# Performance work log

Measured on AMD Instinct MI355X. Metric: run time of the kernel, lower is better.

## Reference

```python
import jax, jax.numpy as jnp
import numpy as np
import math

D_MODEL = 2048
NUM_HEADS = 16
D_K = D_MODEL // NUM_HEADS  # 128
THETA = 10000.0
BATCH = 2
SEQ = 2048


def setup_inputs() -> dict:
    key = jax.random.key(0)
    k1, k2, k3 = jax.random.split(key, 3)
    std_qkv = math.sqrt(2.0 / (D_MODEL + 3 * D_MODEL))
    std_o = math.sqrt(2.0 / (D_MODEL + D_MODEL))
    return {
        "x": jax.random.normal(k1, (BATCH, SEQ, D_MODEL), dtype=jnp.float32),
        "token_positions": jnp.arange(SEQ, dtype=jnp.int64 if jax.config.jax_enable_x64 else jnp.int32),
        "Wqkv": jax.random.normal(k2, (3 * D_MODEL, D_MODEL), dtype=jnp.float32) * std_qkv,
        "Wo": jax.random.normal(k3, (D_MODEL, D_MODEL), dtype=jnp.float32) * std_o,
    }


def _rope(x, positions):
    # x: [b, h, t, d_k]; interleaved even/odd rotation as in the torch module
    half = D_K // 2
    inv_freq = 1.0 / (THETA ** (jnp.arange(half, dtype=x.dtype) / half))
    ang = positions.astype(x.dtype)[:, None] * inv_freq[None, :]  # [t, half]
    sin, cos = jnp.sin(ang), jnp.cos(ang)                          # broadcast over b,h
    x_even, x_odd = x[..., 0::2], x[..., 1::2]
    rot_even = x_even * cos - x_odd * sin
    rot_odd = x_even * sin + x_odd * cos
    return jnp.stack([rot_even, rot_odd], axis=-1).reshape(x.shape)


def reference(x, token_positions, Wqkv, Wo):
    B, T, _ = x.shape
    qkv = x @ Wqkv.T                                  # [b, t, 3*d_model]
    q, k, v = jnp.split(qkv, 3, axis=-1)
    def to_heads(t):
        return t.reshape(B, T, NUM_HEADS, D_K).transpose(0, 2, 1, 3)  # b h t d
    q, k, v = to_heads(q), to_heads(k), to_heads(v)
    q = _rope(q, token_positions)
    k = _rope(k, token_positions)
    scale = 1.0 / math.sqrt(D_K)
    scores = jnp.einsum("bhqd,bhkd->bhqk", q, k) * scale
    causal = jnp.tril(jnp.ones((T, T), dtype=bool))
    scores = jnp.where(causal, scores, jnp.finfo(scores.dtype).min)
    attn = jax.nn.softmax(scores, axis=-1)
    out = jnp.einsum("bhqk,bhkd->bhqd", attn, v)
    out = out.transpose(0, 2, 1, 3).reshape(B, T, D_MODEL)
    return out @ Wo.T
```

## Files before the change

### kernel.cpp

```cpp
#include <hip/hip_runtime.h>
#include <math.h>
#include <stdint.h>

#define NHEADS 16
#define DK 128
#define TSEQ 2048
#define DMODEL 2048

typedef __attribute__((ext_vector_type(8))) short short8;
typedef __attribute__((ext_vector_type(4))) float floatx4;

__device__ __forceinline__ float bf2f(unsigned short h) {
    return __uint_as_float(((unsigned int)h) << 16);
}
__device__ __forceinline__ unsigned short f2bf(float f) {
    unsigned int u = __float_as_uint(f);
    u += 0x7FFFu + ((u >> 16) & 1u);
    return (unsigned short)(u >> 16);
}
__device__ __forceinline__ void async16(unsigned short* lds, const unsigned short* g) {
    __builtin_amdgcn_global_load_lds(
        (const __attribute__((address_space(1))) uint32_t*)g,
        (__attribute__((address_space(3))) uint32_t*)lds, 16, 0, 0);
}

#define NX8 1048576
#define NW8 1572864
#define NO8 524288
__global__ __launch_bounds__(256) void cast_all_bf16(
    const float* __restrict__ x, const float* __restrict__ wqkv, const float* __restrict__ wo,
    unsigned short* __restrict__ xb, unsigned short* __restrict__ wqkvb, unsigned short* __restrict__ wob)
{
    const int i = blockIdx.x * 256 + threadIdx.x;
    const float* src; unsigned short* dst; int k;
    if (i < NX8)            { src = x;    dst = xb;    k = i; }
    else if (i < NX8 + NW8) { src = wqkv; dst = wqkvb; k = i - NX8; }
    else                    { src = wo;   dst = wob;   k = i - NX8 - NW8; }
    const float4* p4 = reinterpret_cast<const float4*>(src) + 2 * (size_t)k;
    const float4 a = p4[0], b = p4[1];
    uint32_t w0 = (uint32_t)f2bf(a.x) | ((uint32_t)f2bf(a.y) << 16);
    uint32_t w1 = (uint32_t)f2bf(a.z) | ((uint32_t)f2bf(a.w) << 16);
    uint32_t w2 = (uint32_t)f2bf(b.x) | ((uint32_t)f2bf(b.y) << 16);
    uint32_t w3 = (uint32_t)f2bf(b.z) | ((uint32_t)f2bf(b.w) << 16);
    uint4 o; o.x = w0; o.y = w1; o.z = w2; o.w = w3;
    *reinterpret_cast<uint4*>(dst + 8 * (size_t)k) = o;
}

__global__ __launch_bounds__(256) void rope_table_kernel(
    const int* __restrict__ pos, float2* __restrict__ tab)
{
    const int idx = blockIdx.x * 256 + threadIdx.x;
    const int tt = idx >> 6, i = idx & 63;
    const double inv_freq = exp(-log(10000.0) * (double)i / 64.0);
    const double ang = (double)pos[tt] * inv_freq;
    tab[idx] = make_float2((float)cos(ang), (float)sin(ang));
}

__global__ __launch_bounds__(512, 1) void gemm_qkv_8ph(
    const unsigned short* __restrict__ A, const unsigned short* __restrict__ B,
    unsigned short* __restrict__ qkvb, unsigned short* __restrict__ vt,
    const float2* __restrict__ tab)
{
    const int K = DMODEL, N = 3 * DMODEL;
    __shared__ unsigned short As[2][256 * 64];
    __shared__ unsigned short Bs[2][192 * 64];

    const int t = threadIdx.x;
    const int lane = t & 63, w = t >> 6;
    const int wr = w >> 2, wc = w & 3;
    const int lr = lane & 15, hi = lane >> 4;

    const int bid = (int)blockIdx.x;
    const int xcd = bid & 7, local = bid >> 3;
    const int row0 = (local & 15) * 256;
    const int col0 = ((xcd << 2) | (local >> 4)) * 192;

    const int rr = t >> 3;
    const int cc = ((t & 7) ^ (rr & 7)) << 3;
    const unsigned short* aP = A + (size_t)(row0 + rr) * K + cc;
    const unsigned short* bP = B + (size_t)(col0 + rr) * K + cc;
    const size_t rstep = (size_t)64 * K;

    floatx4 acc[8][3];
#pragma unroll
    for (int m = 0; m < 8; m++)
#pragma unroll
        for (int n = 0; n < 3; n++)
#pragma unroll
            for (int e = 0; e < 4; e++) acc[m][n][e] = 0.f;

#define STAGE_A(nb, k0n) do { \
        async16(&As[nb][t * 8],          aP + (k0n)); \
        async16(&As[nb][(t + 512) * 8],  aP + rstep + (k0n)); \
        async16(&As[nb][(t + 1024) * 8], aP + 2 * rstep + (k0n)); \
        async16(&As[nb][(t + 1536) * 8], aP + 3 * rstep + (k0n)); \
    } while (0)
#define STAGE_B(nb, k0n) do { \
        async16(&Bs[nb][t * 8],          bP + (k0n)); \
        async16(&Bs[nb][(t + 512) * 8],  bP + rstep + (k0n)); \
        async16(&Bs[nb][(t + 1024) * 8], bP + 2 * rstep + (k0n)); \
    } while (0)

    const int NT = K >> 6;
    const int ch0 = (hi ^ (lr & 7)) * 8;
    const int ch1 = ((4 + hi) ^ (lr & 7)) * 8;

    short8 av0[4][2], av1[4][2], bv[3][2];

#define RD_A(dst, Ac, mh) do { \
        _Pragma("unroll") \
        for (int m = 0; m < 4; m++) { \
            const int ar = (wr * 128 + (mh) * 64 + m * 16 + lr) * 64; \
            dst[m][0] = *(const short8*)&(Ac)[ar + ch0]; \
            dst[m][1] = *(const short8*)&(Ac)[ar + ch1]; \
        } \
    } while (0)
#define RD_B(Bc) do { \
        _Pragma("unroll") \
        for (int n = 0; n < 3; n++) { \
            const int br = (wc * 48 + n * 16 + lr) * 64; \
            bv[n][0] = *(const short8*)&(Bc)[br + ch0]; \
            bv[n][1] = *(const short8*)&(Bc)[br + ch1]; \
        } \
    } while (0)

    STAGE_A(0, 0);
    STAGE_B(0, 0);
    asm volatile("s_waitcnt vmcnt(0)" ::: "memory");
    __builtin_amdgcn_s_barrier();
    RD_A(av0, &As[0][0], 0);
    RD_B(&Bs[0][0]);

    for (int kt = 0; kt < NT; ++kt) {
        const int cur = kt & 1;
        const unsigned short* __restrict__ Ac = &As[cur][0];
        const unsigned short* __restrict__ Bc = &Bs[cur][0];
        const unsigned short* __restrict__ An = &As[cur ^ 1][0];
        const unsigned short* __restrict__ Bn = &Bs[cur ^ 1][0];
        const bool more = (kt + 1 < NT);

        if (more) STAGE_A(cur ^ 1, (kt + 1) << 6);
        RD_A(av1, Ac, 1);
        asm volatile("s_waitcnt lgkmcnt(8)" ::: "memory");
        __builtin_amdgcn_sched_barrier(0);
        __builtin_amdgcn_s_setprio(1);
#pragma unroll
        for (int m = 0; m < 4; m++)
#pragma unroll
            for (int n = 0; n < 3; n++) {
                acc[m][n] = __builtin_amdgcn_mfma_f32_16x16x32_bf16(av0[m][0], bv[n][0], acc[m][n], 0, 0, 0);
                acc[m][n] = __builtin_amdgcn_mfma_f32_16x16x32_bf16(av0[m][1], bv[n][1], acc[m][n], 0, 0, 0);
            }
        __builtin_amdgcn_s_setprio(0);

        if (more) STAGE_B(cur ^ 1, (kt + 1) << 6);
        asm volatile("s_waitcnt lgkmcnt(0)" ::: "memory");
        __builtin_amdgcn_sched_barrier(0);
        __builtin_amdgcn_s_setprio(1);
#pragma unroll
        for (int m = 0; m < 4; m++)
#pragma unroll
            for (int n = 0; n < 3; n++) {
                acc[4 + m][n] = __builtin_amdgcn_mfma_f32_16x16x32_bf16(av1[m][0], bv[n][0], acc[4 + m][n], 0, 0, 0);
                acc[4 + m][n] = __builtin_amdgcn_mfma_f32_16x16x32_bf16(av1[m][1], bv[n][1], acc[4 + m][n], 0, 0, 0);
            }
        __builtin_amdgcn_s_setprio(0);

        if (more) {
            asm volatile("s_waitcnt vmcnt(0)" ::: "memory");
            __builtin_amdgcn_s_barrier();
            RD_A(av0, An, 0);
            RD_B(Bn);
        }
    }
#undef STAGE_A
#undef STAGE_B
#undef RD_A
#undef RD_B

    const int par = lr & 1;
#pragma unroll
    for (int mi = 0; mi < 8; mi++) {
        const int row = row0 + wr * 128 + mi * 16 + hi * 4;
        const int tt = row & (TSEQ - 1);
        const int bb = row >> 11;
#pragma unroll
        for (int ni = 0; ni < 3; ni++) {
            const int col = col0 + wc * 48 + ni * 16 + lr;
            if (col < 2 * DMODEL) {
                const int pi = (col & 127) >> 1;
#pragma unroll
                for (int j = 0; j < 4; j++) {
                    const float2 cs = tab[(tt + j) * 64 + pi];
                    const float v = acc[mi][ni][j];
                    const float p = __shfl_xor(v, 1, 64);
                    const float o = par ? (p * cs.y + v * cs.x)
                                        : (v * cs.x - p * cs.y);
                    qkvb[(size_t)(row + j) * N + col] = f2bf(o);
                }
            } else {
                const int vcol = col - 2 * DMODEL;
                const int h = vcol >> 7, d = vcol & 127;
                uint2 pw;
                pw.x = (uint32_t)f2bf(acc[mi][ni][0]) | ((uint32_t)f2bf(acc[mi][ni][1]) << 16);
                pw.y = (uint32_t)f2bf(acc[mi][ni][2]) | ((uint32_t)f2bf(acc[mi][ni][3]) << 16);
                *(uint2*)&vt[(size_t)((bb * NHEADS + h) * DK + d) * TSEQ + tt] = pw;
            }
        }
    }
}

__global__ __launch_bounds__(512, 1) void gemm_o_8ph(
    const unsigned short* __restrict__ A, const unsigned short* __restrict__ B,
    float* __restrict__ C)
{
    const int K = DMODEL, N = DMODEL;
    __shared__ unsigned short As[2][256 * 64];
    __shared__ unsigned short Bs[2][128 * 64];

    const int t = threadIdx.x;
    const int lane = t & 63, w = t >> 6;
    const int wr = w >> 2, wc = w & 3;
    const int lr = lane & 15, hi = lane >> 4;

    const int bid = (int)blockIdx.x;
    const int xcd = bid & 7, local = bid >> 3;
    const int row0 = (local & 15) * 256;
    const int col0 = ((xcd << 1) | (local >> 4)) * 128;

    const int rr = t >> 3;
    const int cc = ((t & 7) ^ (rr & 7)) << 3;
    const unsigned short* aP = A + (size_t)(row0 + rr) * K + cc;
    const unsigned short* bP = B + (size_t)(col0 + rr) * K + cc;
    const size_t rstep = (size_t)64 * K;

    floatx4 acc[8][2];
#pragma unroll
    for (int m = 0; m < 8; m++)
#pragma unroll
        for (int n = 0; n < 2; n++)
#pragma unroll
            for (int e = 0; e < 4; e++) acc[m][n][e] = 0.f;

#define STAGE_A(nb, k0n) do { \
        async16(&As[nb][t * 8],          aP + (k0n)); \
        async16(&As[nb][(t + 512) * 8],  aP + rstep + (k0n)); \
        async16(&As[nb][(t + 1024) * 8], aP + 2 * rstep + (k0n)); \
        async16(&As[nb][(t + 1536) * 8], aP + 3 * rstep + (k0n)); \
    } while (0)
#define STAGE_B(nb, k0n) do { \
        async16(&Bs[nb][t * 8],          bP + (k0n)); \
        async16(&Bs[nb][(t + 512) * 8],  bP + rstep + (k0n)); \
    } while (0)

    const int NT = K >> 6;
    const int ch0 = (hi ^ (lr & 7)) * 8;
    const int ch1 = ((4 + hi) ^ (lr & 7)) * 8;

    short8 av0[4][2], av1[4][2], bv[2][2];

#define RD_A(dst, Ac, mh) do { \
        _Pragma("unroll") \
        for (int m = 0; m < 4; m++) { \
            const int ar = (wr * 128 + (mh) * 64 + m * 16 + lr) * 64; \
            dst[m][0] = *(const short8*)&(Ac)[ar + ch0]; \
            dst[m][1] = *(const short8*)&(Ac)[ar + ch1]; \
        } \
    } while (0)
#define RD_B(Bc) do { \
        _Pragma("unroll") \
        for (int n = 0; n < 2; n++) { \
            const int br = (wc * 32 + n * 16 + lr) * 64; \
            bv[n][0] = *(const short8*)&(Bc)[br + ch0]; \
            bv[n][1] = *(const short8*)&(Bc)[br + ch1]; \
        } \
    } while (0)

    STAGE_A(0, 0);
    STAGE_B(0, 0);
    asm volatile("s_waitcnt vmcnt(0)" ::: "memory");
    __builtin_amdgcn_s_barrier();
    RD_A(av0, &As[0][0], 0);
    RD_B(&Bs[0][0]);

    for (int kt = 0; kt < NT; ++kt) {
        const int cur = kt & 1;
        const unsigned short* __restrict__ Ac = &As[cur][0];
        const unsigned short* __restrict__ An = &As[cur ^ 1][0];
        const unsigned short* __restrict__ Bn = &Bs[cur ^ 1][0];
        const bool more = (kt + 1 < NT);

        if (more) STAGE_A(cur ^ 1, (kt + 1) << 6);
        RD_A(av1, Ac, 1);
        asm volatile("s_waitcnt lgkmcnt(8)" ::: "memory");
        __builtin_amdgcn_sched_barrier(0);
        __builtin_amdgcn_s_setprio(1);
#pragma unroll
        for (int m = 0; m < 4; m++)
#pragma unroll
            for (int n = 0; n < 2; n++) {
                acc[m][n] = __builtin_amdgcn_mfma_f32_16x16x32_bf16(av0[m][0], bv[n][0], acc[m][n], 0, 0, 0);
                acc[m][n] = __builtin_amdgcn_mfma_f32_16x16x32_bf16(av0[m][1], bv[n][1], acc[m][n], 0, 0, 0);
            }
        __builtin_amdgcn_s_setprio(0);

        if (more) STAGE_B(cur ^ 1, (kt + 1) << 6);
        asm volatile("s_waitcnt lgkmcnt(0)" ::: "memory");
        __builtin_amdgcn_sched_barrier(0);
        __builtin_amdgcn_s_setprio(1);
#pragma unroll
        for (int m = 0; m < 4; m++)
#pragma unroll
            for (int n = 0; n < 2; n++) {
                acc[4 + m][n] = __builtin_amdgcn_mfma_f32_16x16x32_bf16(av1[m][0], bv[n][0], acc[4 + m][n], 0, 0, 0);
                acc[4 + m][n] = __builtin_amdgcn_mfma_f32_16x16x32_bf16(av1[m][1], bv[n][1], acc[4 + m][n], 0, 0, 0);
            }
        __builtin_amdgcn_s_setprio(0);

        if (more) {
            asm volatile("s_waitcnt vmcnt(0)" ::: "memory");
            __builtin_amdgcn_s_barrier();
            RD_A(av0, An, 0);
            RD_B(Bn);
        }
    }
#undef STAGE_A
#undef STAGE_B
#undef RD_A
#undef RD_B

#pragma unroll
    for (int mi = 0; mi < 8; mi++) {
        const int row = row0 + wr * 128 + mi * 16 + hi * 4;
#pragma unroll
        for (int ni = 0; ni < 2; ni++) {
            const int col = col0 + wc * 32 + ni * 16 + lr;
#pragma unroll
            for (int j = 0; j < 4; j++)
                C[(size_t)(row + j) * N + col] = acc[mi][ni][j];
        }
    }
}

__global__ __launch_bounds__(256, 2) void attn_mfma2_kernel(
    const unsigned short* __restrict__ qkvb, const unsigned short* __restrict__ vt,
    unsigned short* __restrict__ outb)
{
    __shared__ unsigned short Ks[2][64 * 128];
    __shared__ unsigned short Vs[128 * 64];
    __shared__ unsigned short Ps[4][32 * 64];

    const int t = threadIdx.x;
    const int lane = t & 63, w = t >> 6;
    const int lr = lane & 15, hi = lane >> 4;
    const int bh = blockIdx.y, b = bh >> 4, h = bh & 15;
    const int qc = (int)gridDim.x - 1 - (int)blockIdx.x;
    const int q0 = qc * 128;
    const int q0w = q0 + w * 32;
    const float scale = 0.08838834764831845f;
    const size_t QROW = 3 * DMODEL;

    const unsigned short* kg = qkvb + (size_t)b * TSEQ * QROW + DMODEL + h * DK;
    const unsigned short* vg = vt + (size_t)bh * DK * TSEQ;

    short8 qf[2][4];
    {
        const unsigned short* qbase = qkvb + (size_t)(b * TSEQ + q0w) * QROW + h * DK;
#pragma unroll
        for (int nt = 0; nt < 2; nt++)
#pragma unroll
            for (int ks = 0; ks < 4; ks++) {
                short8 raw = *(const short8*)(qbase + (size_t)(nt * 16 + lr) * QROW + ks * 32 + hi * 8);
                short8 sc;
#pragma unroll
                for (int e = 0; e < 8; e++)
                    sc[e] = (short)f2bf(bf2f((unsigned short)raw[e]) * scale);
                qf[nt][ks] = sc;
            }
    }

    auto stageK = [&](int bufi, int kv0s) {
#pragma unroll
        for (int i = 0; i < 4; i++) {
            const int s = i * 256 + t;
            const int r = s >> 4;
            const int cc = (s & 15) ^ (r & 7);
            async16(&Ks[bufi][s * 8], kg + (size_t)(kv0s + r) * QROW + cc * 8);
        }
    };
    auto stageV = [&](int kv0s) {
#pragma unroll
        for (int i = 0; i < 4; i++) {
            const int s = i * 256 + t;
            const int r = s >> 3;
            const int cc = (s & 7) ^ (r & 7);
            async16(&Vs[s * 8], vg + (size_t)r * TSEQ + kv0s + cc * 8);
        }
    };

    floatx4 accO[2][8];
#pragma unroll
    for (int nt = 0; nt < 2; nt++)
#pragma unroll
        for (int dt = 0; dt < 8; dt++)
#pragma unroll
            for (int e = 0; e < 4; e++) accO[nt][dt][e] = 0.f;
    float mrun[2] = {-1e30f, -1e30f};
    float lrun[2] = {0.f, 0.f};

    const int ntiles = (q0 + 128) / 64;
    int kbuf = 0;

    stageK(0, 0);
    __syncthreads();

    const int pswz = (lr & 7) << 1;

    for (int ti = 0; ti < ntiles; ti++) {
        const int kv0 = ti * 64;
        const bool havK = (ti + 1 < ntiles);
        stageV(kv0);
        if (havK) stageK(kbuf ^ 1, kv0 + 64);

        const bool active = (kv0 <= q0w + 31);
        float al[2] = {1.f, 1.f};

        if (active) {
            floatx4 st[4][2];
#pragma unroll
            for (int mt = 0; mt < 4; mt++)
#pragma unroll
                for (int nt = 0; nt < 2; nt++)
#pragma unroll
                    for (int e = 0; e < 4; e++) st[mt][nt][e] = 0.f;
#pragma unroll
            for (int mt = 0; mt < 4; mt++) {
                const int r = mt * 16 + lr;
#pragma unroll
                for (int ks = 0; ks < 4; ks++) {
                    const int ch = (ks * 4 + hi) ^ (r & 7);
                    const short8 kf = *(const short8*)&Ks[kbuf][(r * 16 + ch) * 8];
                    st[mt][0] = __builtin_amdgcn_mfma_f32_16x16x32_bf16(kf, qf[0][ks], st[mt][0], 0, 0, 0);
                    st[mt][1] = __builtin_amdgcn_mfma_f32_16x16x32_bf16(kf, qf[1][ks], st[mt][1], 0, 0, 0);
                }
            }
            if (kv0 + 63 > q0w) {
#pragma unroll
                for (int nt = 0; nt < 2; nt++) {
                    const int qg = q0w + nt * 16 + lr;
#pragma unroll
                    for (int mt = 0; mt < 4; mt++)
#pragma unroll
                        for (int rg = 0; rg < 4; rg++) {
                            const int kvg = kv0 + mt * 16 + hi * 4 + rg;
                            if (kvg > qg) st[mt][nt][rg] = -1e30f;
                        }
                }
            }
            float pm[2];
#pragma unroll
            for (int nt = 0; nt < 2; nt++) {
                float m = -1e30f;
#pragma unroll
                for (int mt = 0; mt < 4; mt++)
#pragma unroll
                    for (int rg = 0; rg < 4; rg++) m = fmaxf(m, st[mt][nt][rg]);
                m = fmaxf(m, __shfl_xor(m, 16, 64));
                m = fmaxf(m, __shfl_xor(m, 32, 64));
                pm[nt] = m;
            }
            if (__any((pm[0] > mrun[0] + 8.f) || (pm[1] > mrun[1] + 8.f))) {
#pragma unroll
                for (int nt = 0; nt < 2; nt++) {
                    const float mn = fmaxf(mrun[nt], pm[nt]);
                    al[nt] = __expf(mrun[nt] - mn);
                    mrun[nt] = mn;
                }
#pragma unroll
                for (int rg = 0; rg < 4; rg++) {
                    const float a0 = __shfl(al[0], hi * 4 + rg, 64);
                    const float a1 = __shfl(al[1], hi * 4 + rg, 64);
#pragma unroll
                    for (int dt = 0; dt < 8; dt++) {
                        accO[0][dt][rg] *= a0;
                        accO[1][dt][rg] *= a1;
                    }
                }
            }
#pragma unroll
            for (int nt = 0; nt < 2; nt++) {
                float ls = 0.f;
                const int prow = nt * 16 + lr;
#pragma unroll
                for (int mt = 0; mt < 4; mt++) {
                    float pv[4];
#pragma unroll
                    for (int rg = 0; rg < 4; rg++) {
                        pv[rg] = __expf(st[mt][nt][rg] - mrun[nt]);
                        ls += pv[rg];
                    }
                    uint2 pw;
                    pw.x = (uint32_t)f2bf(pv[0]) | ((uint32_t)f2bf(pv[1]) << 16);
                    pw.y = (uint32_t)f2bf(pv[2]) | ((uint32_t)f2bf(pv[3]) << 16);
                    const int chunk = (mt * 4 + hi) ^ pswz;
                    *(uint2*)&Ps[w][prow * 64 + chunk * 4] = pw;
                }
                ls += __shfl_xor(ls, 16, 64);
                ls += __shfl_xor(ls, 32, 64);
                lrun[nt] = lrun[nt] * al[nt] + ls;
            }
        }
        if (havK) asm volatile("s_waitcnt vmcnt(4)" ::: "memory");
        else      asm volatile("s_waitcnt vmcnt(0)" ::: "memory");
        __builtin_amdgcn_s_barrier();

        if (active) {
#pragma unroll
            for (int ks2 = 0; ks2 < 2; ks2++) {
                const int ch0 = ((ks2 * 8 + hi * 2) ^ pswz) * 4;
                const short8 pa0 = *(const short8*)&Ps[w][(0 * 16 + lr) * 64 + ch0];
                const short8 pa1 = *(const short8*)&Ps[w][(1 * 16 + lr) * 64 + ch0];
#pragma unroll
                for (int dt = 0; dt < 8; dt++) {
                    const int r = dt * 16 + lr;
                    const int ch = (ks2 * 4 + hi) ^ (r & 7);
                    const short8 vf = *(const short8*)&Vs[(r * 8 + ch) * 8];
                    accO[0][dt] = __builtin_amdgcn_mfma_f32_16x16x32_bf16(pa0, vf, accO[0][dt], 0, 0, 0);
                    accO[1][dt] = __builtin_amdgcn_mfma_f32_16x16x32_bf16(pa1, vf, accO[1][dt], 0, 0, 0);
                }
            }
        }
        asm volatile("s_waitcnt vmcnt(0)" ::: "memory");
        __builtin_amdgcn_s_barrier();
        kbuf ^= 1;
    }

#pragma unroll
    for (int nt = 0; nt < 2; nt++) {
        const float lv_own = 1.f / lrun[nt];
#pragma unroll
        for (int rg = 0; rg < 4; rg++) {
            const float lv = __shfl(lv_own, hi * 4 + rg, 64);
            unsigned short* orow = outb + (size_t)(b * TSEQ + q0w + nt * 16 + hi * 4 + rg) * DMODEL + h * DK;
#pragma unroll
            for (int dt = 0; dt < 8; dt++)
                orow[dt * 16 + lr] = f2bf(accO[nt][dt][rg] * lv);
        }
    }
}

extern "C" void kernel_launch(void* const* d_in, const int* in_sizes, int n_in,
                              void* d_out, int out_size, void* d_ws, size_t ws_size,
                              hipStream_t stream)
{
    const float* x    = (const float*)d_in[0];
    const int*   pos  = (const int*)d_in[1];
    const float* Wqkv = (const float*)d_in[2];
    const float* Wo   = (const float*)d_in[3];
    float* out = (float*)d_out;

    unsigned short* qkvb  = (unsigned short*)d_ws;
    unsigned short* vtb   = qkvb + (size_t)25165824;
    unsigned short* xb    = vtb + (size_t)8388608;
    unsigned short* attnb = xb;
    unsigned short* wqkvb = xb + (size_t)8388608;
    unsigned short* wob   = wqkvb + (size_t)12582912;
    float2* tab = (float2*)(wob + (size_t)4194304);

    cast_all_bf16<<<12288, 256, 0, stream>>>(x, Wqkv, Wo, xb, wqkvb, wob);
    rope_table_kernel<<<512, 256, 0, stream>>>(pos, tab);

    gemm_qkv_8ph<<<dim3(512), 512, 0, stream>>>(xb, wqkvb, qkvb, vtb, tab);

    attn_mfma2_kernel<<<dim3(16, 32), 256, 0, stream>>>(qkvb, vtb, attnb);

    gemm_o_8ph<<<dim3(256), 512, 0, stream>>>(attnb, wob, out);
}
```

Measured before the change: 285.9 us.

## Restructure GEMM main loops into four-phase ping-pong schedule with staggered prefetch

Both the QKV and output-projection GEMM loops are reorganised into four phases per k-tile. Each phase reads a quarter of the LDS fragments and runs 12 or 8 MFMAs, and the global-to-LDS prefetch is split into pieces interleaved between phases, with barriers between them. This cuts the fragment registers held at once (av/bv halved) and spreads memory issue across the compute, aiming for better overlap or occupancy. In exchange it adds many more barriers per iteration, and the partial vmcnt wait makes correctness depend on exact load ordering.

```diff
diff --git a/kernel.cpp b/kernel.cpp
--- a/kernel.cpp
+++ b/kernel.cpp
@@ -89,13 +89,15 @@
 #pragma unroll
             for (int e = 0; e < 4; e++) acc[m][n][e] = 0.f;
 
-#define STAGE_A(nb, k0n) do { \
+#define STAGE_A0(nb, k0n) do { \
         async16(&As[nb][t * 8],          aP + (k0n)); \
         async16(&As[nb][(t + 512) * 8],  aP + rstep + (k0n)); \
+    } while (0)
+#define STAGE_A1(nb, k0n) do { \
         async16(&As[nb][(t + 1024) * 8], aP + 2 * rstep + (k0n)); \
         async16(&As[nb][(t + 1536) * 8], aP + 3 * rstep + (k0n)); \
     } while (0)
-#define STAGE_B(nb, k0n) do { \
+#define STAGE_B3(nb, k0n) do { \
         async16(&Bs[nb][t * 8],          bP + (k0n)); \
         async16(&Bs[nb][(t + 512) * 8],  bP + rstep + (k0n)); \
         async16(&Bs[nb][(t + 1024) * 8], bP + 2 * rstep + (k0n)); \
@@ -105,78 +107,76 @@
     const int ch0 = (hi ^ (lr & 7)) * 8;
     const int ch1 = ((4 + hi) ^ (lr & 7)) * 8;
 
-    short8 av0[4][2], av1[4][2], bv[3][2];
-
-#define RD_A(dst, Ac, mh) do { \
+    short8 av[4], bv[3];
+
+#define RD_AV(Ac, mh, ch) do { \
         _Pragma("unroll") \
-        for (int m = 0; m < 4; m++) { \
-            const int ar = (wr * 128 + (mh) * 64 + m * 16 + lr) * 64; \
-            dst[m][0] = *(const short8*)&(Ac)[ar + ch0]; \
-            dst[m][1] = *(const short8*)&(Ac)[ar + ch1]; \
-        } \
-    } while (0)
-#define RD_B(Bc) do { \
+        for (int m = 0; m < 4; m++) \
+            av[m] = *(const short8*)&(Ac)[(wr * 128 + (mh) * 64 + m * 16 + lr) * 64 + (ch)]; \
+    } while (0)
+#define RD_BV(Bc, ch) do { \
         _Pragma("unroll") \
-        for (int n = 0; n < 3; n++) { \
-            const int br = (wc * 48 + n * 16 + lr) * 64; \
-            bv[n][0] = *(const short8*)&(Bc)[br + ch0]; \
-            bv[n][1] = *(const short8*)&(Bc)[br + ch1]; \
-        } \
-    } while (0)
-
-    STAGE_A(0, 0);
-    STAGE_B(0, 0);
+        for (int n = 0; n < 3; n++) \
+            bv[n] = *(const short8*)&(Bc)[(wc * 48 + n * 16 + lr) * 64 + (ch)]; \
+    } while (0)
+#define MFMA_Q(mh) do { \
+        _Pragma("unroll") \
+        for (int m = 0; m < 4; m++) \
+            _Pragma("unroll") \
+            for (int n = 0; n < 3; n++) \
+                acc[(mh) * 4 + m][n] = __builtin_amdgcn_mfma_f32_16x16x32_bf16(av[m], bv[n], acc[(mh) * 4 + m][n], 0, 0, 0); \
+    } while (0)
+#define PH_MFMA(mh) do { \
+        asm volatile("s_waitcnt lgkmcnt(0)" ::: "memory"); \
+        __builtin_amdgcn_sched_barrier(0); \
+        __builtin_amdgcn_s_setprio(1); \
+        MFMA_Q(mh); \
+        __builtin_amdgcn_s_setprio(0); \
+        __builtin_amdgcn_s_barrier(); \
+    } while (0)
+
+    STAGE_A0(0, 0); STAGE_A1(0, 0); STAGE_B3(0, 0);
     asm volatile("s_waitcnt vmcnt(0)" ::: "memory");
     __builtin_amdgcn_s_barrier();
-    RD_A(av0, &As[0][0], 0);
-    RD_B(&Bs[0][0]);
 
     for (int kt = 0; kt < NT; ++kt) {
         const int cur = kt & 1;
         const unsigned short* __restrict__ Ac = &As[cur][0];
         const unsigned short* __restrict__ Bc = &Bs[cur][0];
-        const unsigned short* __restrict__ An = &As[cur ^ 1][0];
-        const unsigned short* __restrict__ Bn = &Bs[cur ^ 1][0];
         const bool more = (kt + 1 < NT);
-
-        if (more) STAGE_A(cur ^ 1, (kt + 1) << 6);
-        RD_A(av1, Ac, 1);
-        asm volatile("s_waitcnt lgkmcnt(8)" ::: "memory");
-        __builtin_amdgcn_sched_barrier(0);
-        __builtin_amdgcn_s_setprio(1);
-#pragma unroll
-        for (int m = 0; m < 4; m++)
-#pragma unroll
-            for (int n = 0; n < 3; n++) {
-                acc[m][n] = __builtin_amdgcn_mfma_f32_16x16x32_bf16(av0[m][0], bv[n][0], acc[m][n], 0, 0, 0);
-                acc[m][n] = __builtin_amdgcn_mfma_f32_16x16x32_bf16(av0[m][1], bv[n][1], acc[m][n], 0, 0, 0);
-            }
-        __builtin_amdgcn_s_setprio(0);
-
-        if (more) STAGE_B(cur ^ 1, (kt + 1) << 6);
-        asm volatile("s_waitcnt lgkmcnt(0)" ::: "memory");
-        __builtin_amdgcn_sched_barrier(0);
-        __builtin_amdgcn_s_setprio(1);
-#pragma unroll
-        for (int m = 0; m < 4; m++)
-#pragma unroll
-            for (int n = 0; n < 3; n++) {
-                acc[4 + m][n] = __builtin_amdgcn_mfma_f32_16x16x32_bf16(av1[m][0], bv[n][0], acc[4 + m][n], 0, 0, 0);
-                acc[4 + m][n] = __builtin_amdgcn_mfma_f32_16x16x32_bf16(av1[m][1], bv[n][1], acc[4 + m][n], 0, 0, 0);
-            }
-        __builtin_amdgcn_s_setprio(0);
+        const int nk = (kt + 1) << 6;
 
         if (more) {
+            STAGE_A0(cur ^ 1, nk);
+            asm volatile("s_waitcnt vmcnt(2)" ::: "memory");
+        } else {
             asm volatile("s_waitcnt vmcnt(0)" ::: "memory");
-            __builtin_amdgcn_s_barrier();
-            RD_A(av0, An, 0);
-            RD_B(Bn);
-        }
-    }
-#undef STAGE_A
-#undef STAGE_B
-#undef RD_A
-#undef RD_B
+        }
+        __builtin_amdgcn_s_barrier();
+        RD_AV(Ac, 0, ch0); RD_BV(Bc, ch0);
+        PH_MFMA(0);
+
+        if (more) STAGE_A1(cur ^ 1, nk);
+        RD_AV(Ac, 1, ch0);
+        __builtin_amdgcn_s_barrier();
+        PH_MFMA(1);
+
+        if (more) STAGE_B3(cur ^ 1, nk);
+        RD_AV(Ac, 0, ch1); RD_BV(Bc, ch1);
+        __builtin_amdgcn_s_barrier();
+        PH_MFMA(0);
+
+        RD_AV(Ac, 1, ch1);
+        __builtin_amdgcn_s_barrier();
+        PH_MFMA(1);
+    }
+#undef STAGE_A0
+#undef STAGE_A1
+#undef STAGE_B3
+#undef RD_AV
+#undef RD_BV
+#undef MFMA_Q
+#undef PH_MFMA
 
     const int par = lr & 1;
 #pragma unroll
@@ -242,13 +242,15 @@
 #pragma unroll
             for (int e = 0; e < 4; e++) acc[m][n][e] = 0.f;
 
-#define STAGE_A(nb, k0n) do { \
+#define STAGE_A0(nb, k0n) do { \
         async16(&As[nb][t * 8],          aP + (k0n)); \
         async16(&As[nb][(t + 512) * 8],  aP + rstep + (k0n)); \
+    } while (0)
+#define STAGE_A1(nb, k0n) do { \
         async16(&As[nb][(t + 1024) * 8], aP + 2 * rstep + (k0n)); \
         async16(&As[nb][(t + 1536) * 8], aP + 3 * rstep + (k0n)); \
     } while (0)
-#define STAGE_B(nb, k0n) do { \
+#define STAGE_B2(nb, k0n) do { \
         async16(&Bs[nb][t * 8],          bP + (k0n)); \
         async16(&Bs[nb][(t + 512) * 8],  bP + rstep + (k0n)); \
     } while (0)
@@ -257,77 +259,76 @@
     const int ch0 = (hi ^ (lr & 7)) * 8;
     const int ch1 = ((4 + hi) ^ (lr & 7)) * 8;
 
-    short8 av0[4][2], av1[4][2], bv[2][2];
-
-#define RD_A(dst, Ac, mh) do { \
+    short8 av[4], bv[2];
+
+#define RD_AV(Ac, mh, ch) do { \
         _Pragma("unroll") \
-        for (int m = 0; m < 4; m++) { \
-            const int ar = (wr * 128 + (mh) * 64 + m * 16 + lr) * 64; \
-            dst[m][0] = *(const short8*)&(Ac)[ar + ch0]; \
-            dst[m][1] = *(const short8*)&(Ac)[ar + ch1]; \
-        } \
-    } while (0)
-#define RD_B(Bc) do { \
+        for (int m = 0; m < 4; m++) \
+            av[m] = *(const short8*)&(Ac)[(wr * 128 + (mh) * 64 + m * 16 + lr) * 64 + (ch)]; \
+    } while (0)
+#define RD_BV(Bc, ch) do { \
         _Pragma("unroll") \
-        for (int n = 0; n < 2; n++) { \
-            const int br = (wc * 32 + n * 16 + lr) * 64; \
-            bv[n][0] = *(const short8*)&(Bc)[br + ch0]; \
-            bv[n][1] = *(const short8*)&(Bc)[br + ch1]; \
-        } \
-    } while (0)
-
-    STAGE_A(0, 0);
-    STAGE_B(0, 0);
+        for (int n = 0; n < 2; n++) \
+            bv[n] = *(const short8*)&(Bc)[(wc * 32 + n * 16 + lr) * 64 + (ch)]; \
+    } while (0)
+#define MFMA_Q(mh) do { \
+        _Pragma("unroll") \
+        for (int m = 0; m < 4; m++) \
+            _Pragma("unroll") \
+            for (int n = 0; n < 2; n++) \
+                acc[(mh) * 4 + m][n] = __builtin_amdgcn_mfma_f32_16x16x32_bf16(av[m], bv[n], acc[(mh) * 4 + m][n], 0, 0, 0); \
+    } while (0)
+#define PH_MFMA(mh) do { \
+        asm volatile("s_waitcnt lgkmcnt(0)" ::: "memory"); \
+        __builtin_amdgcn_sched_barrier(0); \
+        __builtin_amdgcn_s_setprio(1); \
+        MFMA_Q(mh); \
+        __builtin_amdgcn_s_setprio(0); \
+        __builtin_amdgcn_s_barrier(); \
+    } while (0)
+
+    STAGE_A0(0, 0); STAGE_A1(0, 0); STAGE_B2(0, 0);
     asm volatile("s_waitcnt vmcnt(0)" ::: "memory");
     __builtin_amdgcn_s_barrier();
-    RD_A(av0, &As[0][0], 0);
-    RD_B(&Bs[0][0]);
 
     for (int kt = 0; kt < NT; ++kt) {
         const int cur = kt & 1;
         const unsigned short* __restrict__ Ac = &As[cur][0];
-        const unsigned short* __restrict__ An = &As[cur ^ 1][0];
-        const unsigned short* __restrict__ Bn = &Bs[cur ^ 1][0];
+        const unsigned short* __restrict__ Bc = &Bs[cur][0];
         const bool more = (kt + 1 < NT);
-
-        if (more) STAGE_A(cur ^ 1, (kt + 1) << 6);
-        RD_A(av1, Ac, 1);
-        asm volatile("s_waitcnt lgkmcnt(8)" ::: "memory");
-        __builtin_amdgcn_sched_barrier(0);
-        __builtin_amdgcn_s_setprio(1);
-#pragma unroll
-        for (int m = 0; m < 4; m++)
-#pragma unroll
-            for (int n = 0; n < 2; n++) {
-                acc[m][n] = __builtin_amdgcn_mfma_f32_16x16x32_bf16(av0[m][0], bv[n][0], acc[m][n], 0, 0, 0);
-                acc[m][n] = __builtin_amdgcn_mfma_f32_16x16x32_bf16(av0[m][1], bv[n][1], acc[m][n], 0, 0, 0);
-            }
-        __builtin_amdgcn_s_setprio(0);
-
-        if (more) STAGE_B(cur ^ 1, (kt + 1) << 6);
-        asm volatile("s_waitcnt lgkmcnt(0)" ::: "memory");
-        __builtin_amdgcn_sched_barrier(0);
-        __builtin_amdgcn_s_setprio(1);
-#pragma unroll
-        for (int m = 0; m < 4; m++)
-#pragma unroll
-            for (int n = 0; n < 2; n++) {
-                acc[4 + m][n] = __builtin_amdgcn_mfma_f32_16x16x32_bf16(av1[m][0], bv[n][0], acc[4 + m][n], 0, 0, 0);
-                acc[4 + m][n] = __builtin_amdgcn_mfma_f32_16x16x32_bf16(av1[m][1], bv[n][1], acc[4 + m][n], 0, 0, 0);
-            }
-        __builtin_amdgcn_s_setprio(0);
+        const int nk = (kt + 1) << 6;
 
         if (more) {
+            STAGE_A0(cur ^ 1, nk);
+            asm volatile("s_waitcnt vmcnt(2)" ::: "memory");
+        } else {
             asm volatile("s_waitcnt vmcnt(0)" ::: "memory");
-            __builtin_amdgcn_s_barrier();
-            RD_A(av0, An, 0);
-            RD_B(Bn);
-        }
-    }
-#undef STAGE_A
-#undef STAGE_B
-#undef RD_A
-#undef RD_B
+        }
+        __builtin_amdgcn_s_barrier();
+        RD_AV(Ac, 0, ch0); RD_BV(Bc, ch0);
+        PH_MFMA(0);
+
+        if (more) STAGE_A1(cur ^ 1, nk);
+        RD_AV(Ac, 1, ch0);
+        __builtin_amdgcn_s_barrier();
+        PH_MFMA(1);
+
+        if (more) STAGE_B2(cur ^ 1, nk);
+        RD_AV(Ac, 0, ch1); RD_BV(Bc, ch1);
+        __builtin_amdgcn_s_barrier();
+        PH_MFMA(0);
+
+        RD_AV(Ac, 1, ch1);
+        __builtin_amdgcn_s_barrier();
+        PH_MFMA(1);
+    }
+#undef STAGE_A0
+#undef STAGE_A1
+#undef STAGE_B2
+#undef RD_AV
+#undef RD_BV
+#undef MFMA_Q
+#undef PH_MFMA
 
 #pragma unroll
     for (int mi = 0; mi < 8; mi++) {
```

After: 353.1 us. 23.5% more time.
